# Kernel tuning notes

Hardware: AMD Instinct MI355X
Metric: run time of the kernel (lower is better)

The kernel has to match this reference:

```python
import math
import jax, jax.numpy as jnp
import numpy as np

B, L, H = 32, 1024, 128

def setup_inputs() -> dict:
    key = jax.random.key(0)
    k1, k2, k3, k4 = jax.random.split(key, 4)
    a = jax.random.normal(k1, (B, L, H), dtype=jnp.float32)
    b = jax.random.normal(k2, (B, L, H), dtype=jnp.float32)
    mask_a = jax.random.randint(k3, (B, L, 1), 0, 2, dtype=jnp.int32)
    mask_b = jax.random.randint(k4, (B, L, 1), 0, 2, dtype=jnp.int32)
    temperature = jnp.asarray(1.0 / math.sqrt(H), dtype=jnp.float32)
    return {"a": a, "b": b, "mask_a": mask_a, "mask_b": mask_b, "temperature": temperature}

def reference(a, b, mask_a, mask_b, temperature):
    # scores: [B, La, Lb]
    scores = jnp.einsum('bld,bmd->blm', a, b) * temperature
    # outer product of token validity masks -> pair mask [B, La, Lb]
    mask = jnp.einsum('blk,bmk->blm', mask_a.astype(jnp.float32), mask_b.astype(jnp.float32)) > 0
    scores = jnp.where(mask, scores, jnp.float32(-10000.0))
    attention_a = jax.nn.softmax(scores, axis=1)  # normalize over La (columns)
    attention_b = jax.nn.softmax(scores, axis=2)  # normalize over Lb (rows)
    feature_a = jnp.einsum('blm,bmd->bld', attention_b, b)
    feature_b = jnp.einsum('blm,bmd->bld', attention_a, a)  # valid since La == Lb
    return (feature_a, feature_b)
```

## Files before the change

kernel.cpp:

```cpp
#include <hip/hip_runtime.h>
#include <math.h>

#define BN 32
#define LL 1024
#define HH 128

typedef __attribute__((ext_vector_type(8))) short short8;
typedef __attribute__((ext_vector_type(4))) float f32x4;

static const size_t SZ_BF = (size_t)BN * LL * HH * 2;

__device__ __forceinline__ ushort f2bf(float x) {
  union { float f; unsigned u; } c; c.f = x;
  unsigned r = c.u + 0x7fffu + ((c.u >> 16) & 1u);
  return (ushort)(r >> 16);
}
__device__ __forceinline__ float bf2f(ushort h) {
  union { unsigned u; float f; } c; c.u = ((unsigned)h) << 16;
  return c.f;
}
__device__ __forceinline__ short8 ld8(const ushort* p) {
  return *(const short8*)p;
}

__global__ __launch_bounds__(256) void k_convert(
    const float* __restrict__ a, const float* __restrict__ b,
    const int* __restrict__ mask_b,
    ushort* __restrict__ abf, ushort* __restrict__ bbf,
    ushort* __restrict__ aT, ushort* __restrict__ bT,
    float* __restrict__ meanb, float* __restrict__ invmean) {
  int bb = blockIdx.y;
  int l0 = blockIdx.x * 64;
  int which = blockIdx.z;
  const float* src = which ? b : a;
  ushort* dst  = which ? bbf : abf;
  ushort* dstT = which ? bT : aT;
  float* dmean = which ? meanb : invmean;
  __shared__ __align__(16) ushort T[128][72];
  __shared__ float accS[128];
  __shared__ float wgt[64];
  int t = threadIdx.x;
  if (t < 128) accS[t] = 0.f;
  if (t < 64)
    wgt[t] = which ? 1.0f : ((mask_b[bb * LL + l0 + t] == 0) ? 1.0f : 0.0f);
  int lrow = t >> 5;
  int dcol = (t & 31) * 4;
#pragma unroll
  for (int p = 0; p < 8; ++p) {
    int l = p * 8 + lrow;
    float4 v = *(const float4*)&src[((size_t)bb * LL + l0 + l) * HH + dcol];
    ushort4 u;
    u.x = f2bf(v.x); u.y = f2bf(v.y); u.z = f2bf(v.z); u.w = f2bf(v.w);
    *(ushort4*)&dst[((size_t)bb * LL + l0 + l) * HH + dcol] = u;
    T[dcol + 0][l] = u.x; T[dcol + 1][l] = u.y;
    T[dcol + 2][l] = u.z; T[dcol + 3][l] = u.w;
  }
  __syncthreads();
  int drow = t >> 3;
  int c8 = (t & 7) * 8;
#pragma unroll
  for (int q = 0; q < 4; ++q) {
    int d = q * 32 + drow;
    short8 val = *(const short8*)&T[d][c8];
    *(short8*)&dstT[((size_t)bb * HH + d) * LL + l0 + c8] = val;
    float s = 0.f;
#pragma unroll
    for (int j = 0; j < 8; ++j) s += wgt[c8 + j] * bf2f((ushort)val[j]);
    atomicAdd(&accS[d], s);
  }
  __syncthreads();
  if (t < 128) atomicAdd(&dmean[bb * HH + t], accS[t]);
}

__global__ __launch_bounds__(256, 4) void k_colsum(
    const ushort* __restrict__ abf, const ushort* __restrict__ bbf,
    const int* __restrict__ mask_a, const int* __restrict__ mask_b,
    const float* __restrict__ temp_p, ushort* __restrict__ aT) {
  int wg = blockIdx.x;
  int bb = wg & 31;
  int m0 = (wg >> 5) * 32;
  int t = threadIdx.x;
  int w = t >> 6, lane = t & 63, l16 = lane & 15, quad = lane >> 4;
  float temp = temp_p[0];
  __shared__ float biasA[LL];
  __shared__ float csred[4][2][16];
  __shared__ float invs[32];
  for (int i = t; i < LL; i += 256)
    biasA[i] = mask_a[bb * LL + i] ? 0.0f : -10000.0f;

  short8 Bm[2][4];
  float biasB[2];
#pragma unroll
  for (int mt = 0; mt < 2; ++mt) {
    int m = m0 + mt * 16 + l16;
    biasB[mt] = mask_b[bb * LL + m] ? 0.0f : -10000.0f;
#pragma unroll
    for (int k = 0; k < 4; ++k)
      Bm[mt][k] = ld8(&bbf[((size_t)bb * LL + m) * HH + k * 32 + quad * 8]);
  }
  __syncthreads();

  short8 Al[4];
  {
    const ushort* arow = &abf[((size_t)bb * LL + w * 256 + l16) * HH];
#pragma unroll
    for (int k = 0; k < 4; ++k) Al[k] = ld8(&arow[k * 32 + quad * 8]);
  }
  float cs[2] = {0.f, 0.f};
  for (int it = 0; it < 16; ++it) {
    int lbase = w * 256 + it * 16;
    short8 AlN[4];
    {
      int itn = (it + 1) & 15;
      const ushort* arow = &abf[((size_t)bb * LL + w * 256 + itn * 16 + l16) * HH];
#pragma unroll
      for (int k = 0; k < 4; ++k) AlN[k] = ld8(&arow[k * 32 + quad * 8]);
    }
#pragma unroll
    for (int mt = 0; mt < 2; ++mt) {
      f32x4 sacc = {0.f, 0.f, 0.f, 0.f};
#pragma unroll
      for (int k = 0; k < 4; ++k)
        sacc = __builtin_amdgcn_mfma_f32_16x16x32_bf16(Al[k], Bm[mt][k], sacc, 0, 0, 0);
#pragma unroll
      for (int r = 0; r < 4; ++r) {
        int l = lbase + quad * 4 + r;
        cs[mt] += __expf(sacc[r] * temp + biasA[l] + biasB[mt]);
      }
    }
#pragma unroll
    for (int k = 0; k < 4; ++k) Al[k] = AlN[k];
  }
#pragma unroll
  for (int mt = 0; mt < 2; ++mt) {
    cs[mt] += __shfl_xor(cs[mt], 16);
    cs[mt] += __shfl_xor(cs[mt], 32);
  }
  if (lane < 16) {
#pragma unroll
    for (int mt = 0; mt < 2; ++mt) csred[w][mt][l16] = cs[mt];
  }
  __syncthreads();
  if (t < 32) {
    float s = csred[0][t >> 4][t & 15] + csred[1][t >> 4][t & 15] +
              csred[2][t >> 4][t & 15] + csred[3][t >> 4][t & 15];
    invs[t] = s > 0.f ? 1.0f / s : 0.0f;
  }
  __syncthreads();
  {
    int ml = t & 31;
    float iv = invs[ml];
    for (int d = t >> 5; d < HH; d += 8) {
      size_t idx = ((size_t)bb * HH + d) * LL + m0 + ml;
      aT[idx] = f2bf(bf2f(aT[idx]) * iv);
    }
  }
}

__global__ __launch_bounds__(256, 2) void k_features(
    const ushort* __restrict__ abf, const ushort* __restrict__ bbf,
    const ushort* __restrict__ aS, const ushort* __restrict__ bT,
    const int* __restrict__ mask_a, const int* __restrict__ mask_b,
    const float* __restrict__ temp_p, const float* __restrict__ meanb,
    const float* __restrict__ invmean, float* __restrict__ out) {
  int wg = blockIdx.x;
  int bb = wg & 31;
  int l0 = (wg >> 5) * 64;
  int t = threadIdx.x;
  int w = t >> 6, lane = t & 63, l16 = lane & 15, quad = lane >> 4;
  float temp = temp_p[0];

  __shared__ float biasBs[LL];
  __shared__ __align__(16) ushort Pa[2][64 * 72];
  __shared__ float rspart[4][64];
  __shared__ float rsfin[64];

  for (int i = t; i < LL; i += 256)
    biasBs[i] = mask_b[bb * LL + i] ? 0.0f : -10000.0f;

  float biasA_lt[4];
  short8 Afix[4][4];
#pragma unroll
  for (int lt = 0; lt < 4; ++lt) {
    int l = l0 + lt * 16 + l16;
    biasA_lt[lt] = mask_a[bb * LL + l] ? 0.0f : -10000.0f;
#pragma unroll
    for (int k = 0; k < 4; ++k)
      Afix[lt][k] = ld8(&abf[((size_t)bb * LL + l) * HH + k * 32 + quad * 8]);
  }

  f32x4 accA[4][2], accB[4][2];
  f32x4 zero = {0.f, 0.f, 0.f, 0.f};
#pragma unroll
  for (int lt = 0; lt < 4; ++lt)
#pragma unroll
    for (int dt = 0; dt < 2; ++dt) { accA[lt][dt] = zero; accB[lt][dt] = zero; }
  float rs_lt[4] = {0.f, 0.f, 0.f, 0.f};
  __syncthreads();

  short8 Am[4];
  {
    const ushort* brow = &bbf[((size_t)bb * LL + w * 16 + l16) * HH];
#pragma unroll
    for (int k = 0; k < 4; ++k) Am[k] = ld8(&brow[k * 32 + quad * 8]);
  }

  int buf = 0;
  for (int m0 = 0; m0 < LL; m0 += 64) {
    short8 Bb[2][2], Bs[2][2];
#pragma unroll
    for (int dt = 0; dt < 2; ++dt) {
      size_t drow = (size_t)bb * HH + w * 32 + dt * 16 + l16;
      const ushort* btrow = &bT[drow * LL + m0];
      const ushort* asrow = &aS[drow * LL + m0];
#pragma unroll
      for (int ks = 0; ks < 2; ++ks) {
        Bb[dt][ks] = ld8(&btrow[ks * 32 + quad * 8]);
        Bs[dt][ks] = ld8(&asrow[ks * 32 + quad * 8]);
      }
    }
    float bB[4];
#pragma unroll
    for (int r = 0; r < 4; ++r) bB[r] = biasBs[m0 + w * 16 + quad * 4 + r];

    ushort* pa = &Pa[buf][0];
#pragma unroll
    for (int lt = 0; lt < 4; ++lt) {
      f32x4 sacc = zero;
#pragma unroll
      for (int k = 0; k < 4; ++k)
        sacc = __builtin_amdgcn_mfma_f32_16x16x32_bf16(Am[k], Afix[lt][k], sacc, 0, 0, 0);
      ushort pav[4];
#pragma unroll
      for (int r = 0; r < 4; ++r) {
        pav[r] = f2bf(__expf(sacc[r] * temp + biasA_lt[lt] + bB[r]));
        rs_lt[lt] += bf2f(pav[r]);
      }
      uint2 ka;
      ka.x = (uint)pav[0] | ((uint)pav[1] << 16);
      ka.y = (uint)pav[2] | ((uint)pav[3] << 16);
      *(uint2*)&pa[(lt * 16 + l16) * 72 + w * 16 + quad * 4] = ka;
    }

    {
      int mn = (m0 + 64) & (LL - 1);
      const ushort* brow = &bbf[((size_t)bb * LL + mn + w * 16 + l16) * HH];
#pragma unroll
      for (int k = 0; k < 4; ++k) Am[k] = ld8(&brow[k * 32 + quad * 8]);
    }

    __syncthreads();

#pragma unroll
    for (int lt = 0; lt < 4; ++lt) {
#pragma unroll
      for (int ks = 0; ks < 2; ++ks) {
        short8 PaF = *(const short8*)&pa[(lt * 16 + l16) * 72 + ks * 32 + quad * 8];
#pragma unroll
        for (int dt = 0; dt < 2; ++dt) {
          accA[lt][dt] = __builtin_amdgcn_mfma_f32_16x16x32_bf16(PaF, Bb[dt][ks], accA[lt][dt], 0, 0, 0);
          accB[lt][dt] = __builtin_amdgcn_mfma_f32_16x16x32_bf16(PaF, Bs[dt][ks], accB[lt][dt], 0, 0, 0);
        }
      }
    }
    buf ^= 1;
  }

#pragma unroll
  for (int lt = 0; lt < 4; ++lt) {
    rs_lt[lt] += __shfl_xor(rs_lt[lt], 16);
    rs_lt[lt] += __shfl_xor(rs_lt[lt], 32);
  }
  if (lane < 16) {
#pragma unroll
    for (int lt = 0; lt < 4; ++lt) rspart[w][lt * 16 + l16] = rs_lt[lt];
  }
  __syncthreads();
  if (t < 64)
    rsfin[t] = rspart[0][t] + rspart[1][t] + rspart[2][t] + rspart[3][t];
  __syncthreads();

  float* outA = out;
  float* outB = out + (size_t)BN * LL * HH;
#pragma unroll
  for (int dt = 0; dt < 2; ++dt) {
    int d = w * 32 + dt * 16 + l16;
    float mb = meanb[bb * HH + d] * (1.0f / 1024.0f);
    float im = invmean[bb * HH + d] * (1.0f / 1024.0f);
#pragma unroll
    for (int lt = 0; lt < 4; ++lt) {
#pragma unroll
      for (int r = 0; r < 4; ++r) {
        int l = lt * 16 + quad * 4 + r;
        float rsv = rsfin[l];
        float fa = (rsv > 0.f) ? accA[lt][dt][r] / rsv : mb;
        float fb = accB[lt][dt][r] + im;
        outA[((size_t)bb * LL + l0 + l) * HH + d] = fa;
        outB[((size_t)bb * LL + l0 + l) * HH + d] = fb;
      }
    }
  }
}

extern "C" void kernel_launch(void* const* d_in, const int* in_sizes, int n_in,
                              void* d_out, int out_size, void* d_ws, size_t ws_size,
                              hipStream_t stream) {
  const float* a = (const float*)d_in[0];
  const float* b = (const float*)d_in[1];
  const int* mask_a = (const int*)d_in[2];
  const int* mask_b = (const int*)d_in[3];
  const float* temp = (const float*)d_in[4];
  float* out = (float*)d_out;

  char* wsb = (char*)d_ws;
  ushort* abf = (ushort*)(wsb + 0 * SZ_BF);
  ushort* bbf = (ushort*)(wsb + 1 * SZ_BF);
  ushort* aT  = (ushort*)(wsb + 2 * SZ_BF);
  ushort* bT  = (ushort*)(wsb + 3 * SZ_BF);
  float* meanb   = (float*)(wsb + 4 * SZ_BF);
  float* invmean = meanb + BN * HH;

  hipMemsetAsync(meanb, 0, 2 * BN * HH * sizeof(float), stream);
  k_convert<<<dim3(16, 32, 2), 256, 0, stream>>>(a, b, mask_b, abf, bbf, aT, bT,
                                                 meanb, invmean);
  k_colsum<<<dim3(1024), 256, 0, stream>>>(abf, bbf, mask_a, mask_b, temp, aT);
  k_features<<<dim3(512), 256, 0, stream>>>(abf, bbf, aT, bT, mask_a, mask_b,
                                            temp, meanb, invmean, out);
  (void)in_sizes; (void)n_in; (void)out_size; (void)ws_size;
}
```

Measured before the change: 193.4 us.

## Move column-scaling of aT into separate vectorized kernel and retile Pa LDS layout

The colsum kernel now writes only the per-column inverse sums to a small buffer, and a new k_scale kernel rescales aT with coalesced 16-byte loads and stores. Previously each colsum workgroup did scattered 2-byte read-modify-writes strided by LL across aT. Separately, the Pa shared-memory tile in k_features changes from padded row-major to a fragment-major layout, so each MFMA operand read becomes a contiguous short8 load. The cost is an extra kernel launch and one more full pass over aT.

```diff
diff --git a/kernel.cpp b/kernel.cpp
--- a/kernel.cpp
+++ b/kernel.cpp
@@ -75,7 +75,7 @@
 __global__ __launch_bounds__(256, 4) void k_colsum(
     const ushort* __restrict__ abf, const ushort* __restrict__ bbf,
     const int* __restrict__ mask_a, const int* __restrict__ mask_b,
-    const float* __restrict__ temp_p, ushort* __restrict__ aT) {
+    const float* __restrict__ temp_p, float* __restrict__ invc) {
   int wg = blockIdx.x;
   int bb = wg & 31;
   int m0 = (wg >> 5) * 32;
@@ -84,7 +84,6 @@
   float temp = temp_p[0];
   __shared__ float biasA[LL];
   __shared__ float csred[4][2][16];
-  __shared__ float invs[32];
   for (int i = t; i < LL; i += 256)
     biasA[i] = mask_a[bb * LL + i] ? 0.0f : -10000.0f;
 
@@ -144,17 +143,28 @@
   if (t < 32) {
     float s = csred[0][t >> 4][t & 15] + csred[1][t >> 4][t & 15] +
               csred[2][t >> 4][t & 15] + csred[3][t >> 4][t & 15];
-    invs[t] = s > 0.f ? 1.0f / s : 0.0f;
-  }
-  __syncthreads();
-  {
-    int ml = t & 31;
-    float iv = invs[ml];
-    for (int d = t >> 5; d < HH; d += 8) {
-      size_t idx = ((size_t)bb * HH + d) * LL + m0 + ml;
-      aT[idx] = f2bf(bf2f(aT[idx]) * iv);
-    }
-  }
+    invc[bb * LL + m0 + t] = s > 0.f ? 1.0f / s : 0.0f;
+  }
+}
+
+__global__ __launch_bounds__(256) void k_scale(
+    ushort* __restrict__ aT, const float* __restrict__ invc) {
+  size_t base = ((size_t)blockIdx.x * 256 + threadIdx.x) * 8;
+  int b = (int)(base >> 17);
+  int m = (int)(base & (LL - 1));
+  short8 v = *(short8*)&aT[base];
+  float4 i0 = *(const float4*)&invc[b * LL + m];
+  float4 i1 = *(const float4*)&invc[b * LL + m + 4];
+  short8 o;
+  o[0] = (short)f2bf(bf2f((ushort)v[0]) * i0.x);
+  o[1] = (short)f2bf(bf2f((ushort)v[1]) * i0.y);
+  o[2] = (short)f2bf(bf2f((ushort)v[2]) * i0.z);
+  o[3] = (short)f2bf(bf2f((ushort)v[3]) * i0.w);
+  o[4] = (short)f2bf(bf2f((ushort)v[4]) * i1.x);
+  o[5] = (short)f2bf(bf2f((ushort)v[5]) * i1.y);
+  o[6] = (short)f2bf(bf2f((ushort)v[6]) * i1.z);
+  o[7] = (short)f2bf(bf2f((ushort)v[7]) * i1.w);
+  *(short8*)&aT[base] = o;
 }
 
 __global__ __launch_bounds__(256, 2) void k_features(
@@ -171,7 +181,7 @@
   float temp = temp_p[0];
 
   __shared__ float biasBs[LL];
-  __shared__ __align__(16) ushort Pa[2][64 * 72];
+  __shared__ __align__(16) ushort Pa[2][4096];
   __shared__ float rspart[4][64];
   __shared__ float rsfin[64];
 
@@ -204,6 +214,10 @@
 #pragma unroll
     for (int k = 0; k < 4; ++k) Am[k] = ld8(&brow[k * 32 + quad * 8]);
   }
+
+  int ks_w = w >> 1;
+  int qf = ((w & 1) << 1) + (quad >> 1);
+  int jb = (quad & 1) << 2;
 
   int buf = 0;
   for (int m0 = 0; m0 < LL; m0 += 64) {
@@ -239,7 +253,8 @@
       uint2 ka;
       ka.x = (uint)pav[0] | ((uint)pav[1] << 16);
       ka.y = (uint)pav[2] | ((uint)pav[3] << 16);
-      *(uint2*)&pa[(lt * 16 + l16) * 72 + w * 16 + quad * 4] = ka;
+      int pidx = (((lt * 2 + ks_w) * 4 + qf) * 16 + l16) * 8 + jb;
+      *(uint2*)&pa[pidx] = ka;
     }
 
     {
@@ -255,7 +270,8 @@
     for (int lt = 0; lt < 4; ++lt) {
 #pragma unroll
       for (int ks = 0; ks < 2; ++ks) {
-        short8 PaF = *(const short8*)&pa[(lt * 16 + l16) * 72 + ks * 32 + quad * 8];
+        int ridx = (((lt * 2 + ks) * 4 + quad) * 16 + l16) * 8;
+        short8 PaF = *(const short8*)&pa[ridx];
 #pragma unroll
         for (int dt = 0; dt < 2; ++dt) {
           accA[lt][dt] = __builtin_amdgcn_mfma_f32_16x16x32_bf16(PaF, Bb[dt][ks], accA[lt][dt], 0, 0, 0);
@@ -317,13 +333,15 @@
   ushort* bbf = (ushort*)(wsb + 1 * SZ_BF);
   ushort* aT  = (ushort*)(wsb + 2 * SZ_BF);
   ushort* bT  = (ushort*)(wsb + 3 * SZ_BF);
-  float* meanb   = (float*)(wsb + 4 * SZ_BF);
+  float* invc = (float*)(wsb + 4 * SZ_BF);
+  float* meanb   = invc + (size_t)BN * LL;
   float* invmean = meanb + BN * HH;
 
   hipMemsetAsync(meanb, 0, 2 * BN * HH * sizeof(float), stream);
   k_convert<<<dim3(16, 32, 2), 256, 0, stream>>>(a, b, mask_b, abf, bbf, aT, bT,
                                                  meanb, invmean);
-  k_colsum<<<dim3(1024), 256, 0, stream>>>(abf, bbf, mask_a, mask_b, temp, aT);
+  k_colsum<<<dim3(1024), 256, 0, stream>>>(abf, bbf, mask_a, mask_b, temp, invc);
+  k_scale<<<dim3(2048), 256, 0, stream>>>(aT, invc);
   k_features<<<dim3(512), 256, 0, stream>>>(abf, bbf, aT, bT, mask_a, mask_b,
                                             temp, meanb, invmean, out);
   (void)in_sizes; (void)n_in; (void)out_size; (void)ws_size;
```

New measurement: 194.7 us. No clear change (+0.7%).
